# Optimization experiments

Hardware: AMD Instinct MI355X
Metric: run time of the kernel (lower is better)

## Reference

```python
import jax, jax.numpy as jnp
import numpy as np

N_NODES = 100000
N_EDGES = 600000
IN_FEATS = 128
HIDDEN = 128


def sage_conv(x, src, dst, w_l, b_l, w_r, num_nodes):
    """PyG SAGEConv with mean aggregation.
    out = mean_{j in N(i)} x_j @ w_l.T + b_l + x_i @ w_r.T
    src/dst: int arrays [E]; messages flow src -> dst.
    """
    msgs = x[src]                                             # [E, F] gather
    summed = jax.ops.segment_sum(msgs, dst, num_segments=num_nodes)  # [N, F]
    ones = jnp.ones((src.shape[0],), dtype=x.dtype)
    deg = jax.ops.segment_sum(ones, dst, num_segments=num_nodes)     # [N]
    agg = summed / jnp.maximum(deg, 1.0)[:, None]             # mean, safe for deg=0
    return agg @ w_l.T + b_l + x @ w_r.T


def setup_inputs() -> dict:
    key = jax.random.key(0)
    ks = jax.random.split(key, 10)

    def glorot(k, shape):
        fan_in = shape[-1]
        bound = 1.0 / np.sqrt(fan_in)
        return jax.random.uniform(k, shape, jnp.float32, -bound, bound)

    x = jax.random.normal(ks[0], (N_NODES, IN_FEATS), dtype=jnp.float32)
    xedge = jax.random.randint(ks[1], (2, N_EDGES), 0, N_NODES, dtype=jnp.int64)
    return {
        "x": x,
        "xedge": xedge,
        # SAGEConv 1 (in_feats -> hidden): lin_l (with bias) + lin_r (no bias)
        "w1_l": glorot(ks[2], (HIDDEN, IN_FEATS)),
        "b1_l": glorot(ks[3], (HIDDEN,)),
        "w1_r": glorot(ks[4], (HIDDEN, IN_FEATS)),
        # SAGEConv 2 (hidden -> hidden)
        "w2_l": glorot(ks[5], (HIDDEN, HIDDEN)),
        "b2_l": glorot(ks[6], (HIDDEN,)),
        "w2_r": glorot(ks[7], (HIDDEN, HIDDEN)),
        # Decoder: Linear(hidden -> hidden)
        "w_dec": glorot(ks[8], (HIDDEN, HIDDEN)),
        "b_dec": glorot(ks[9], (HIDDEN,)),
    }


def reference(x, xedge, w1_l, b1_l, w1_r, w2_l, b2_l, w2_r, w_dec, b_dec):
    src, dst = xedge[0], xedge[1]
    n = x.shape[0]
    h = sage_conv(x, src, dst, w1_l, b1_l, w1_r, n)   # conv1
    h = jax.nn.relu(h)
    # dropout omitted (deterministic eval semantics)
    h = sage_conv(h, src, dst, w2_l, b2_l, w2_r, n)   # conv2 -> encoder output
    dx = h @ w_dec.T + b_dec                          # decoder
    return (h, dx)
```

## Files before the change

### kernel.cpp

```cpp
#include <hip/hip_runtime.h>

typedef __attribute__((ext_vector_type(8))) short bf16x8;
typedef __attribute__((ext_vector_type(4))) float f32x4;
typedef unsigned int uint;
typedef unsigned short ushort;

#define NFEAT 128

__device__ __forceinline__ ushort f2b(float f) {
    uint u = __float_as_uint(f);
    u = (u + 0x7fffu + ((u >> 16) & 1u)) >> 16;
    return (ushort)u;
}

__global__ __launch_bounds__(256) void prep(
    const float* __restrict__ x, ushort* __restrict__ x_bf, long nx,
    const float* __restrict__ w1l, const float* __restrict__ w1r,
    const float* __restrict__ w2l, const float* __restrict__ w2r,
    const float* __restrict__ wd,
    ushort* __restrict__ wc1, ushort* __restrict__ wc2, ushort* __restrict__ wdec,
    const int* __restrict__ dst, int* __restrict__ deg, int E, int nCvt)
{
    const int b = blockIdx.x;
    if (b < nCvt) {
        long i = ((long)b * 256 + threadIdx.x) * 4;
        if (i < nx) {
            float4 v = *(const float4*)(x + i);
            ushort4 o;
            o.x = f2b(v.x); o.y = f2b(v.y); o.z = f2b(v.z); o.w = f2b(v.w);
            *(ushort4*)(x_bf + i) = o;
        }
    } else if (b < nCvt + 256) {
        const int bb = b - nCvt;
        const int i = (bb & 127) * 256 + threadIdx.x;
        const int row = i >> 8, col = i & 255;
        const float* wl = (bb < 128) ? w1l : w2l;
        const float* wr = (bb < 128) ? w1r : w2r;
        ushort* dstw = (bb < 128) ? wc1 : wc2;
        float v = (col < 128) ? wl[row * 128 + col] : wr[row * 128 + col - 128];
        dstw[i] = f2b(v);
    } else if (b < nCvt + 320) {
        const int i = (b - nCvt - 256) * 256 + threadIdx.x;
        wdec[i] = f2b(wd[i]);
    } else {
        const int e = (b - nCvt - 320) * 256 + threadIdx.x;
        if (e < E) atomicAdd(&deg[dst[e]], 1);
    }
}

__global__ __launch_bounds__(256) void scan_blocks(const int* __restrict__ in, int* __restrict__ out,
                                                   int* __restrict__ bsum, int n) {
    __shared__ int lds[256];
    const int t = threadIdx.x;
    const int base = blockIdx.x * 1024 + t * 4;
    int a[4];
#pragma unroll
    for (int q = 0; q < 4; ++q) a[q] = (base + q < n) ? in[base + q] : 0;
    const int tsum = a[0] + a[1] + a[2] + a[3];
    lds[t] = tsum;
    __syncthreads();
    for (int off = 1; off < 256; off <<= 1) {
        int v = (t >= off) ? lds[t - off] : 0;
        __syncthreads();
        lds[t] += v;
        __syncthreads();
    }
    const int excl = lds[t] - tsum;
    if (t == 255) bsum[blockIdx.x] = lds[255];
    int r = excl;
#pragma unroll
    for (int q = 0; q < 4; ++q) {
        if (base + q < n) out[base + q] = r;
        r += a[q];
    }
}

__global__ __launch_bounds__(256) void scan_carry(int* __restrict__ bsum, int nb) {
    __shared__ int lds[256];
    const int t = threadIdx.x;
    const int v = (t < nb) ? bsum[t] : 0;
    lds[t] = v;
    __syncthreads();
    for (int off = 1; off < 256; off <<= 1) {
        int u = (t >= off) ? lds[t - off] : 0;
        __syncthreads();
        lds[t] += u;
        __syncthreads();
    }
    if (t < nb) bsum[t] = lds[t] - v;
}

__global__ void scan_add(int* __restrict__ row_off, int* __restrict__ pos,
                         const int* __restrict__ bsum, int n, int E) {
    const int i = blockIdx.x * blockDim.x + threadIdx.x;
    if (i < n) {
        const int v = row_off[i] + bsum[i >> 10];
        row_off[i] = v;
        pos[i] = v;
    }
    if (i == 0) row_off[n] = E;
}

__global__ void fill_csr(const int* __restrict__ src, const int* __restrict__ dst,
                         int* __restrict__ pos, int* __restrict__ perm, int E) {
    const int e = blockIdx.x * blockDim.x + threadIdx.x;
    if (e < E) {
        const int p = atomicAdd(&pos[dst[e]], 1);
        perm[p] = src[e];
    }
}

__global__ __launch_bounds__(256) void gather_mean_bf(const int* __restrict__ row_off,
                                                      const int* __restrict__ perm,
                                                      const ushort* __restrict__ feat,
                                                      ushort* __restrict__ out, int n) {
    const int node = (blockIdx.x * 256 + threadIdx.x) >> 4;
    if (node >= n) return;
    const int chunk = threadIdx.x & 15;
    const int lo = row_off[node], hi = row_off[node + 1];
    float acc[8] = {0.f, 0.f, 0.f, 0.f, 0.f, 0.f, 0.f, 0.f};
    int i = lo;
    for (; i + 3 < hi; i += 4) {
        const int s0 = perm[i], s1 = perm[i + 1], s2 = perm[i + 2], s3 = perm[i + 3];
        const uint4 v0 = *(const uint4*)(feat + (size_t)s0 * NFEAT + chunk * 8);
        const uint4 v1 = *(const uint4*)(feat + (size_t)s1 * NFEAT + chunk * 8);
        const uint4 v2 = *(const uint4*)(feat + (size_t)s2 * NFEAT + chunk * 8);
        const uint4 v3 = *(const uint4*)(feat + (size_t)s3 * NFEAT + chunk * 8);
        const uint p0[4] = {v0.x, v0.y, v0.z, v0.w};
        const uint p1[4] = {v1.x, v1.y, v1.z, v1.w};
        const uint p2[4] = {v2.x, v2.y, v2.z, v2.w};
        const uint p3[4] = {v3.x, v3.y, v3.z, v3.w};
#pragma unroll
        for (int q = 0; q < 4; ++q) {
            acc[2 * q]     += __uint_as_float(p0[q] << 16) + __uint_as_float(p1[q] << 16)
                            + __uint_as_float(p2[q] << 16) + __uint_as_float(p3[q] << 16);
            acc[2 * q + 1] += __uint_as_float(p0[q] & 0xffff0000u) + __uint_as_float(p1[q] & 0xffff0000u)
                            + __uint_as_float(p2[q] & 0xffff0000u) + __uint_as_float(p3[q] & 0xffff0000u);
        }
    }
    for (; i < hi; ++i) {
        const int s = perm[i];
        const uint4 v = *(const uint4*)(feat + (size_t)s * NFEAT + chunk * 8);
        const uint p[4] = {v.x, v.y, v.z, v.w};
#pragma unroll
        for (int q = 0; q < 4; ++q) {
            acc[2 * q]     += __uint_as_float(p[q] << 16);
            acc[2 * q + 1] += __uint_as_float(p[q] & 0xffff0000u);
        }
    }
    const float inv = 1.0f / fmaxf((float)(hi - lo), 1.0f);
    ushort o[8] __attribute__((aligned(16)));
#pragma unroll
    for (int q = 0; q < 8; ++q) o[q] = f2b(acc[q] * inv);
    *(uint4*)(out + (size_t)node * NFEAT + chunk * 8) = *(const uint4*)o;
}

template <bool RELU, bool DEC>
__global__ __launch_bounds__(256) void sage_mfma(
    const ushort* __restrict__ Amean, const ushort* __restrict__ Axin,
    const ushort* __restrict__ Wcat, const float* __restrict__ bias,
    const ushort* __restrict__ Wdec, const float* __restrict__ bdec,
    float* __restrict__ outf, ushort* __restrict__ outb,
    float* __restrict__ dxp, int n)
{
    __shared__ uint4 smem4[2048];
    char* As = (char*)smem4;
    char* Ws = As + 16384;
    const int t = threadIdx.x;
    const int m0 = blockIdx.x * 128;
    const int lane = t & 63;
    const int wid = t >> 6;
    const int lrow = lane & 15;
    const int lq = lane >> 4;

    f32x4 acc[2][8];
#pragma unroll
    for (int m = 0; m < 2; ++m)
#pragma unroll
        for (int nn = 0; nn < 8; ++nn) acc[m][nn] = (f32x4){0.f, 0.f, 0.f, 0.f};

    for (int kt = 0; kt < 4; ++kt) {
        const ushort* Abase = (kt < 2) ? Amean : Axin;
        const int co = (kt & 1) * 64;
#pragma unroll
        for (int i = 0; i < 4; ++i) {
            const int c = t + i * 256;
            const int row = c >> 3, cL = c & 7;
            const int gm = m0 + row;
            uint4 v = make_uint4(0, 0, 0, 0);
            if (gm < n) v = *(const uint4*)((const char*)Abase + ((size_t)gm * NFEAT + co) * 2 + cL * 16);
            *(uint4*)(As + row * 128 + ((cL * 16) ^ ((row & 7) << 4))) = v;
        }
#pragma unroll
        for (int i = 0; i < 4; ++i) {
            const int c = t + i * 256;
            const int row = c >> 3, cL = c & 7;
            const uint4 v = *(const uint4*)((const char*)Wcat + ((size_t)row * 256 + kt * 64) * 2 + cL * 16);
            *(uint4*)(Ws + row * 128 + ((cL * 16) ^ ((row & 7) << 4))) = v;
        }
        __syncthreads();
#pragma unroll
        for (int ks = 0; ks < 2; ++ks) {
            bf16x8 af[2], bfr[8];
#pragma unroll
            for (int m = 0; m < 2; ++m) {
                const int row = wid * 32 + m * 16 + lrow;
                af[m] = *(const bf16x8*)(As + row * 128 + (((ks * 4 + lq) * 16) ^ ((row & 7) << 4)));
            }
#pragma unroll
            for (int nn = 0; nn < 8; ++nn) {
                const int row = nn * 16 + lrow;
                bfr[nn] = *(const bf16x8*)(Ws + row * 128 + (((ks * 4 + lq) * 16) ^ ((row & 7) << 4)));
            }
#pragma unroll
            for (int m = 0; m < 2; ++m)
#pragma unroll
                for (int nn = 0; nn < 8; ++nn)
                    acc[m][nn] = __builtin_amdgcn_mfma_f32_16x16x32_bf16(bfr[nn], af[m], acc[m][nn], 0, 0, 0);
        }
        __syncthreads();
    }
    char* Lh = As;
#pragma unroll
    for (int m = 0; m < 2; ++m) {
        const int row = wid * 32 + m * 16 + lrow;
        const int grow = m0 + row;
#pragma unroll
        for (int nn = 0; nn < 8; ++nn) {
            const int colb = nn * 16 + lq * 4;
            const float4 bv = *(const float4*)(bias + colb);
            float v0 = acc[m][nn][0] + bv.x;
            float v1 = acc[m][nn][1] + bv.y;
            float v2 = acc[m][nn][2] + bv.z;
            float v3 = acc[m][nn][3] + bv.w;
            if (RELU) {
                v0 = fmaxf(v0, 0.f); v1 = fmaxf(v1, 0.f);
                v2 = fmaxf(v2, 0.f); v3 = fmaxf(v3, 0.f);
            }
            ushort4 ob;
            ob.x = f2b(v0); ob.y = f2b(v1); ob.z = f2b(v2); ob.w = f2b(v3);
            if (grow < n) {
                if (outf) *(float4*)(outf + (size_t)grow * NFEAT + colb) = make_float4(v0, v1, v2, v3);
                if (outb) *(ushort4*)(outb + (size_t)grow * NFEAT + colb) = ob;
            }
            if (DEC)
                *(ushort4*)(Lh + row * 256 + ((colb * 2) ^ ((row & 7) << 4))) = ob;
        }
    }
    if (DEC) {
        f32x4 acc2[2][8];
#pragma unroll
        for (int m = 0; m < 2; ++m)
#pragma unroll
            for (int nn = 0; nn < 8; ++nn) acc2[m][nn] = (f32x4){0.f, 0.f, 0.f, 0.f};
#pragma unroll
        for (int ks = 0; ks < 4; ++ks) {
            bf16x8 af2[2], bf2[8];
#pragma unroll
            for (int m = 0; m < 2; ++m) {
                const int row = wid * 32 + m * 16 + lrow;
                af2[m] = *(const bf16x8*)(Lh + row * 256 + ((ks * 64 + lq * 16) ^ ((row & 7) << 4)));
            }
#pragma unroll
            for (int nn = 0; nn < 8; ++nn)
                bf2[nn] = *(const bf16x8*)(Wdec + (size_t)(nn * 16 + lrow) * NFEAT + ks * 32 + lq * 8);
#pragma unroll
            for (int m = 0; m < 2; ++m)
#pragma unroll
                for (int nn = 0; nn < 8; ++nn)
                    acc2[m][nn] = __builtin_amdgcn_mfma_f32_16x16x32_bf16(bf2[nn], af2[m], acc2[m][nn], 0, 0, 0);
        }
#pragma unroll
        for (int m = 0; m < 2; ++m) {
            const int grow = m0 + wid * 32 + m * 16 + lrow;
            if (grow < n) {
#pragma unroll
                for (int nn = 0; nn < 8; ++nn) {
                    const int colb = nn * 16 + lq * 4;
                    const float4 bv = *(const float4*)(bdec + colb);
                    *(float4*)(dxp + (size_t)grow * NFEAT + colb) =
                        make_float4(acc2[m][nn][0] + bv.x, acc2[m][nn][1] + bv.y,
                                    acc2[m][nn][2] + bv.z, acc2[m][nn][3] + bv.w);
                }
            }
        }
    }
}

extern "C" void kernel_launch(void* const* d_in, const int* in_sizes, int n_in,
                              void* d_out, int out_size, void* d_ws, size_t ws_size,
                              hipStream_t stream) {
    const float* x     = (const float*)d_in[0];
    const int*   xedge = (const int*)d_in[1];
    const float* w1_l  = (const float*)d_in[2];
    const float* b1_l  = (const float*)d_in[3];
    const float* w1_r  = (const float*)d_in[4];
    const float* w2_l  = (const float*)d_in[5];
    const float* b2_l  = (const float*)d_in[6];
    const float* w2_r  = (const float*)d_in[7];
    const float* w_dec = (const float*)d_in[8];
    const float* b_dec = (const float*)d_in[9];

    const int N = in_sizes[0] / NFEAT;
    const int E = in_sizes[1] / 2;
    const int* src = xedge;
    const int* dst = xedge + E;

    float* h_out = (float*)d_out;
    float* dxp   = h_out + (size_t)N * NFEAT;

    char* ws = (char*)d_ws;
    ushort* x_bf    = (ushort*)ws;
    ushort* h1_bf   = x_bf   + (size_t)N * NFEAT;
    ushort* mean_bf = h1_bf  + (size_t)N * NFEAT;
    ushort* wc1     = mean_bf + (size_t)N * NFEAT;
    ushort* wc2     = wc1 + 128 * 256;
    ushort* wdec    = wc2 + 128 * 256;
    int* deg        = (int*)(wdec + 128 * 128);
    int* row_off    = deg + N;
    int* pos        = row_off + (N + 1);
    int* bsum       = pos + N;
    int* perm       = bsum + 256;

    hipMemsetAsync(deg, 0, (size_t)N * sizeof(int), stream);
    const long nx = (long)N * NFEAT;
    const int nCvt = (int)((nx / 4 + 255) / 256);
    const int histB = (E + 255) / 256;
    prep<<<nCvt + 320 + histB, 256, 0, stream>>>(x, x_bf, nx, w1_l, w1_r, w2_l, w2_r, w_dec,
                                                 wc1, wc2, wdec, dst, deg, E, nCvt);

    const int nb = (N + 1023) / 1024;
    scan_blocks<<<nb, 256, 0, stream>>>(deg, row_off, bsum, N);
    scan_carry<<<1, 256, 0, stream>>>(bsum, nb);
    scan_add<<<(N + 255) / 256, 256, 0, stream>>>(row_off, pos, bsum, N, E);
    fill_csr<<<histB, 256, 0, stream>>>(src, dst, pos, perm, E);

    const int gb = (N + 127) / 128;
    const int ggb = (N * 16 + 255) / 256;

    gather_mean_bf<<<ggb, 256, 0, stream>>>(row_off, perm, x_bf, mean_bf, N);
    sage_mfma<true, false><<<gb, 256, 0, stream>>>(mean_bf, x_bf, wc1, b1_l,
                                                   nullptr, nullptr, nullptr, h1_bf, nullptr, N);

    gather_mean_bf<<<ggb, 256, 0, stream>>>(row_off, perm, h1_bf, mean_bf, N);
    sage_mfma<false, true><<<gb, 256, 0, stream>>>(mean_bf, h1_bf, wc2, b2_l,
                                                   wdec, b_dec, h_out, nullptr, dxp, N);

    (void)n_in; (void)out_size; (void)ws_size;
}
```

Baseline: 209.3 us.

## Load MFMA operands directly from global and fold scan carry into scan_add

The SAGE MFMA kernel no longer stages the A and W tiles through LDS with barriers. Each lane now loads its bf16x8 fragments straight from global memory, with the row index clamped for the tail, and shared memory is kept only for the decoder stage. Separately, the single-block scan_carry kernel is removed: each scan_add wave sums the preceding block totals with a shuffle reduction, saving one launch. The cost is redundant global and L2 traffic for the weights and possibly uncoalesced fragment loads, in exchange for dropping LDS round trips and syncs.

```diff
diff --git a/kernel.cpp b/kernel.cpp
--- a/kernel.cpp
+++ b/kernel.cpp
@@ -75,28 +75,20 @@
     }
 }
 
-__global__ __launch_bounds__(256) void scan_carry(int* __restrict__ bsum, int nb) {
-    __shared__ int lds[256];
-    const int t = threadIdx.x;
-    const int v = (t < nb) ? bsum[t] : 0;
-    lds[t] = v;
-    __syncthreads();
-    for (int off = 1; off < 256; off <<= 1) {
-        int u = (t >= off) ? lds[t - off] : 0;
-        __syncthreads();
-        lds[t] += u;
-        __syncthreads();
-    }
-    if (t < nb) bsum[t] = lds[t] - v;
-}
-
-__global__ void scan_add(int* __restrict__ row_off, int* __restrict__ pos,
-                         const int* __restrict__ bsum, int n, int E) {
-    const int i = blockIdx.x * blockDim.x + threadIdx.x;
+__global__ __launch_bounds__(256) void scan_add(int* __restrict__ row_off, int* __restrict__ pos,
+                                                const int* __restrict__ bsum, int n, int E) {
+    const int i = blockIdx.x * 256 + threadIdx.x;
+    const int cb = blockIdx.x >> 2;
+    const int lane = threadIdx.x & 63;
+    int v = 0;
+    if (lane < cb) v += bsum[lane];
+    if (lane + 64 < cb) v += bsum[lane + 64];
+#pragma unroll
+    for (int off = 1; off < 64; off <<= 1) v += __shfl_xor(v, off);
     if (i < n) {
-        const int v = row_off[i] + bsum[i >> 10];
-        row_off[i] = v;
-        pos[i] = v;
+        const int r = row_off[i] + v;
+        row_off[i] = r;
+        pos[i] = r;
     }
     if (i == 0) row_off[n] = E;
 }
@@ -163,9 +155,8 @@
     float* __restrict__ outf, ushort* __restrict__ outb,
     float* __restrict__ dxp, int n)
 {
-    __shared__ uint4 smem4[2048];
-    char* As = (char*)smem4;
-    char* Ws = As + 16384;
+    __shared__ uint4 LhBuf[DEC ? 2048 : 1];
+    char* Lh = (char*)LhBuf;
     const int t = threadIdx.x;
     const int m0 = blockIdx.x * 128;
     const int lane = t & 63;
@@ -173,54 +164,41 @@
     const int lrow = lane & 15;
     const int lq = lane >> 4;
 
+    int ar[2];
+#pragma unroll
+    for (int m = 0; m < 2; ++m) {
+        int r = m0 + wid * 32 + m * 16 + lrow;
+        ar[m] = (r < n) ? r : (n - 1);
+    }
+
     f32x4 acc[2][8];
 #pragma unroll
     for (int m = 0; m < 2; ++m)
 #pragma unroll
         for (int nn = 0; nn < 8; ++nn) acc[m][nn] = (f32x4){0.f, 0.f, 0.f, 0.f};
 
+#pragma unroll
     for (int kt = 0; kt < 4; ++kt) {
         const ushort* Abase = (kt < 2) ? Amean : Axin;
         const int co = (kt & 1) * 64;
 #pragma unroll
-        for (int i = 0; i < 4; ++i) {
-            const int c = t + i * 256;
-            const int row = c >> 3, cL = c & 7;
-            const int gm = m0 + row;
-            uint4 v = make_uint4(0, 0, 0, 0);
-            if (gm < n) v = *(const uint4*)((const char*)Abase + ((size_t)gm * NFEAT + co) * 2 + cL * 16);
-            *(uint4*)(As + row * 128 + ((cL * 16) ^ ((row & 7) << 4))) = v;
-        }
-#pragma unroll
-        for (int i = 0; i < 4; ++i) {
-            const int c = t + i * 256;
-            const int row = c >> 3, cL = c & 7;
-            const uint4 v = *(const uint4*)((const char*)Wcat + ((size_t)row * 256 + kt * 64) * 2 + cL * 16);
-            *(uint4*)(Ws + row * 128 + ((cL * 16) ^ ((row & 7) << 4))) = v;
-        }
-        __syncthreads();
-#pragma unroll
         for (int ks = 0; ks < 2; ++ks) {
+            const int kcol = co + ks * 32 + lq * 8;
             bf16x8 af[2], bfr[8];
 #pragma unroll
-            for (int m = 0; m < 2; ++m) {
-                const int row = wid * 32 + m * 16 + lrow;
-                af[m] = *(const bf16x8*)(As + row * 128 + (((ks * 4 + lq) * 16) ^ ((row & 7) << 4)));
-            }
-#pragma unroll
-            for (int nn = 0; nn < 8; ++nn) {
-                const int row = nn * 16 + lrow;
-                bfr[nn] = *(const bf16x8*)(Ws + row * 128 + (((ks * 4 + lq) * 16) ^ ((row & 7) << 4)));
-            }
+            for (int m = 0; m < 2; ++m)
+                af[m] = *(const bf16x8*)(Abase + (size_t)ar[m] * NFEAT + kcol);
+#pragma unroll
+            for (int nn = 0; nn < 8; ++nn)
+                bfr[nn] = *(const bf16x8*)(Wcat + (size_t)(nn * 16 + lrow) * 256 + kt * 64 + ks * 32 + lq * 8);
 #pragma unroll
             for (int m = 0; m < 2; ++m)
 #pragma unroll
                 for (int nn = 0; nn < 8; ++nn)
                     acc[m][nn] = __builtin_amdgcn_mfma_f32_16x16x32_bf16(bfr[nn], af[m], acc[m][nn], 0, 0, 0);
         }
-        __syncthreads();
-    }
-    char* Lh = As;
+    }
+
 #pragma unroll
     for (int m = 0; m < 2; ++m) {
         const int row = wid * 32 + m * 16 + lrow;
@@ -331,7 +309,6 @@
 
     const int nb = (N + 1023) / 1024;
     scan_blocks<<<nb, 256, 0, stream>>>(deg, row_off, bsum, N);
-    scan_carry<<<1, 256, 0, stream>>>(bsum, nb);
     scan_add<<<(N + 255) / 256, 256, 0, stream>>>(row_off, pos, bsum, N, E);
     fill_csr<<<histB, 256, 0, stream>>>(src, dst, pos, perm, E);
 
```

New measurement: 245.0 us. +17.1%, slower.
